# Kernel tuning notes

Measured on AMD Instinct MI355X. Metric: run time of the kernel, lower is better.

## Reference

```python
import jax, jax.numpy as jnp
import numpy as np

N = 100_000      # nodes
E = 1_600_000    # edges (before self loops)
IN = 128         # in_dim
HID = 64         # hidden_dim (per head)
HEADS = 2
NEG_SLOPE = 0.2  # PyG GATConv default negative_slope


def setup_inputs() -> dict:
    key = jax.random.key(0)
    k = jax.random.split(key, 6)
    x = jax.random.normal(k[0], (N, IN), jnp.float32)
    edge_index = jax.random.randint(k[1], (2, E), 0, N, dtype=jnp.int64)
    # GATConv linear (no bias in lin, bias added after aggregation in PyG)
    W = jax.random.normal(k[2], (IN, HEADS * HID), jnp.float32) * (1.0 / np.sqrt(IN))
    att_src = jax.random.normal(k[3], (HEADS, HID), jnp.float32) * 0.1
    att_dst = jax.random.normal(k[4], (HEADS, HID), jnp.float32) * 0.1
    bias = jnp.zeros((HEADS * HID,), jnp.float32)
    prelu_w = jnp.full((HEADS * HID,), 0.25, jnp.float32)  # nn.PReLU default init
    return {"x": x, "edge_index": edge_index, "W": W, "att_src": att_src,
            "att_dst": att_dst, "bias": bias, "prelu_w": prelu_w}


def reference(x, edge_index, W, att_src, att_dst, bias, prelu_w):
    n = x.shape[0]
    h = (x @ W).reshape(n, HEADS, HID)                 # [N,H,C]
    a_s = jnp.einsum('nhc,hc->nh', h, att_src)         # [N,H]
    a_d = jnp.einsum('nhc,hc->nh', h, att_dst)         # [N,H]
    # add self loops (PyG default add_self_loops=True)
    loops = jnp.arange(n, dtype=edge_index.dtype)
    src = jnp.concatenate([edge_index[0], loops])      # [Et]
    dst = jnp.concatenate([edge_index[1], loops])      # [Et]
    logits = a_s[src] + a_d[dst]                       # [Et,H]
    logits = jnp.where(logits >= 0, logits, NEG_SLOPE * logits)  # LeakyReLU
    # segment softmax over destination neighborhoods
    m = jax.ops.segment_max(logits, dst, num_segments=n)         # [N,H]
    e = jnp.exp(logits - m[dst])
    s = jax.ops.segment_sum(e, dst, num_segments=n)              # [N,H]
    alpha = e / (s[dst] + 1e-16)                                 # [Et,H]
    # (attention dropout p=0.2 is identity in eval mode)
    msg = h[src] * alpha[..., None]                    # [Et,H,C]
    out = jax.ops.segment_sum(msg, dst, num_segments=n).reshape(n, HEADS * HID)
    out = out + bias
    # PReLU with per-channel weight
    return jnp.where(out >= 0, out, prelu_w * out)
```

## Files before the change

### kernel.cpp

```cpp
#include <hip/hip_runtime.h>
#include <hip/hip_fp16.h>
#include <hip/hip_bf16.h>
#include <cstdint>
#include <cstddef>

#define NEG_SLOPE 0.2f
#define BSH 8
#define BNODES 256
#define CAP 5120
#define SLOTS 48

typedef __attribute__((ext_vector_type(8))) short short8v;
typedef __attribute__((ext_vector_type(4))) float f32x4;

__device__ __forceinline__ uint32_t bf16pair(float a, float b) {
    __hip_bfloat162 h = __float22bfloat162_rn(make_float2(a, b));
    return *reinterpret_cast<uint32_t*>(&h);
}
__device__ __forceinline__ uint16_t rne16(float f) {
    uint32_t u = __float_as_uint(f);
    return (uint16_t)((u + 0x7fffu + ((u >> 16) & 1u)) >> 16);
}
__device__ __forceinline__ float bflo(uint32_t u) { return __uint_as_float(u << 16); }
__device__ __forceinline__ float bfhi(uint32_t u) { return __uint_as_float(u & 0xffff0000u); }

__global__ __launch_bounds__(256, 3) void gemm_scatter(
    const float* __restrict__ x, const float* __restrict__ W,
    const float* __restrict__ att_src, const float* __restrict__ att_dst,
    uint32_t* __restrict__ hb, float* __restrict__ a_s, float* __restrict__ a_d,
    const int* __restrict__ src, const int* __restrict__ dst,
    int* __restrict__ gcur, uint32_t* __restrict__ pairs,
    int e, int nb, int n, int nbs)
{
    constexpr int PW = 136;
    __shared__ __align__(16) char smem[52224];
    const int tid = threadIdx.x;

    if (blockIdx.x < nbs) {
        int* histL  = (int*)smem;
        int* gbaseL = histL + 512;
        const int t0 = blockIdx.x * 4096;

        for (int i = tid; i < nb; i += 256) histL[i] = 0;
        __syncthreads();

        int      myb[16];
        int      myslot[16];
        uint32_t mypk[16];
#pragma unroll 16
        for (int k = 0; k < 16; ++k) {
            int i = t0 + tid + k * 256;
            if (i < e) {
                int s = __builtin_nontemporal_load(src + i);
                int d = __builtin_nontemporal_load(dst + i);
                int b = d >> BSH;
                myb[k]    = b;
                mypk[k]   = (uint32_t)s | ((uint32_t)(d & (BNODES - 1)) << 17);
                myslot[k] = atomicAdd(&histL[b], 1);
            } else myb[k] = -1;
        }
        __syncthreads();
        for (int i = tid; i < nb; i += 256) {
            int c = histL[i];
            gbaseL[i] = c ? atomicAdd(&gcur[i], c) : 0;
        }
        __syncthreads();
#pragma unroll 16
        for (int k = 0; k < 16; ++k) {
            if (myb[k] >= 0) {
                int p = gbaseL[myb[k]] + myslot[k];
                if (p < CAP) pairs[(size_t)myb[k] * CAP + p] = mypk[k];
            }
        }
        return;
    }

    unsigned short* Wt = (unsigned short*)smem;
    unsigned short* Hs = (unsigned short*)(smem + 34816);
    const int w    = tid >> 6;
    const int lane = tid & 63;
    const int cl   = lane & 15;
    const int gq   = lane >> 4;
    const int base = (blockIdx.x - nbs) * 64;

    const float4* W4 = (const float4*)W;
#pragma unroll
    for (int i = 0; i < 8; ++i) {
        int idx = tid + i * 256;
        int k   = (idx >> 5) * 2, c4 = (idx & 31) * 4;
        float4 v0 = W4[k * 32 + (idx & 31)];
        float4 v1 = W4[(k + 1) * 32 + (idx & 31)];
        *(uint32_t*)&Wt[(c4 + 0) * PW + k] = bf16pair(v0.x, v1.x);
        *(uint32_t*)&Wt[(c4 + 1) * PW + k] = bf16pair(v0.y, v1.y);
        *(uint32_t*)&Wt[(c4 + 2) * PW + k] = bf16pair(v0.z, v1.z);
        *(uint32_t*)&Wt[(c4 + 3) * PW + k] = bf16pair(v0.w, v1.w);
    }

    float asr[8], adr[8];
#pragma unroll
    for (int t = 0; t < 8; ++t) {
        asr[t] = att_src[t * 16 + cl];
        adr[t] = att_dst[t * 16 + cl];
    }
    __syncthreads();

    const int rowg = base + w * 16 + cl;
    const int rowc = rowg < n ? rowg : (n - 1);
    const f32x4* xp = (const f32x4*)(x + (size_t)rowc * 128);

    f32x4 acc[8];
#pragma unroll
    for (int t = 0; t < 8; ++t) acc[t] = (f32x4){0.f, 0.f, 0.f, 0.f};

#pragma unroll
    for (int s = 0; s < 4; ++s) {
        int kq = s * 8 + gq * 2;
        f32x4 f0 = __builtin_nontemporal_load(xp + kq);
        f32x4 f1 = __builtin_nontemporal_load(xp + kq + 1);
        union { short8v v; uint32_t d[4]; } A;
        A.d[0] = bf16pair(f0.x, f0.y);
        A.d[1] = bf16pair(f0.z, f0.w);
        A.d[2] = bf16pair(f1.x, f1.y);
        A.d[3] = bf16pair(f1.z, f1.w);
#pragma unroll
        for (int t = 0; t < 8; ++t) {
            union { short8v v; uint4 q; } B;
            B.q = *(const uint4*)&Wt[(t * 16 + cl) * PW + s * 32 + gq * 8];
            acc[t] = __builtin_amdgcn_mfma_f32_16x16x32_bf16(A.v, B.v, acc[t], 0, 0, 0);
        }
    }

    float ps0[4], ps1[4], pd0[4], pd1[4];
#pragma unroll
    for (int r = 0; r < 4; ++r) { ps0[r] = ps1[r] = pd0[r] = pd1[r] = 0.f; }
#pragma unroll
    for (int t = 0; t < 8; ++t) {
#pragma unroll
        for (int r = 0; r < 4; ++r) {
            float v = acc[t][r];
            if (t < 4) { ps0[r] = fmaf(v, asr[t], ps0[r]); pd0[r] = fmaf(v, adr[t], pd0[r]); }
            else       { ps1[r] = fmaf(v, asr[t], ps1[r]); pd1[r] = fmaf(v, adr[t], pd1[r]); }
        }
    }
#pragma unroll
    for (int off = 1; off < 16; off <<= 1) {
#pragma unroll
        for (int r = 0; r < 4; ++r) {
            ps0[r] += __shfl_xor(ps0[r], off);
            ps1[r] += __shfl_xor(ps1[r], off);
            pd0[r] += __shfl_xor(pd0[r], off);
            pd1[r] += __shfl_xor(pd1[r], off);
        }
    }
    if (cl == 0) {
#pragma unroll
        for (int r = 0; r < 4; ++r) {
            int rg = base + w * 16 + gq * 4 + r;
            if (rg < n) {
                a_s[rg * 2 + 0] = ps0[r]; a_s[rg * 2 + 1] = ps1[r];
                a_d[rg * 2 + 0] = pd0[r]; a_d[rg * 2 + 1] = pd1[r];
            }
        }
    }

#pragma unroll
    for (int t = 0; t < 8; ++t) {
#pragma unroll
        for (int r = 0; r < 4; ++r) {
            int row = gq * 4 + r;
            Hs[(size_t)w * 16 * PW + row * PW + t * 16 + cl] = rne16(acc[t][r]);
        }
    }
    __syncthreads();
#pragma unroll
    for (int q = 0; q < 4; ++q) {
        int row = q * 4 + gq;
        int cu  = 4 * cl;
        uint4 v = *(const uint4*)&Hs[(size_t)w * 16 * PW + row * PW + cu * 2];
        int rg = base + w * 16 + row;
        if (rg < n) *(uint4*)&hb[(size_t)rg * 64 + cu] = v;
    }
}

__global__ __launch_bounds__(512) void build_cols(
    const uint32_t* __restrict__ pairs, const int* __restrict__ gcur,
    uint32_t* __restrict__ meta, uint32_t* __restrict__ cols, int n, int nb)
{
    __shared__ int curL[BNODES];
    const int b = blockIdx.x, tid = threadIdx.x;
    const int nbase = b * BNODES;
    const int nodes = min(BNODES, n - nbase);
    const int C = min(gcur[b], CAP);

    if (tid < BNODES) curL[tid] = 1;
    __syncthreads();
    if (tid < nodes)
        cols[(size_t)(nbase + tid) * SLOTS] = (uint32_t)(nbase + tid);

    for (int i = tid; i < C; i += 512) {
        uint32_t p = __builtin_nontemporal_load(pairs + (size_t)b * CAP + i);
        int dl = p >> 17;
        int s  = p & 0x1FFFF;
        int slot = atomicAdd(&curL[dl], 1);
        if (slot < SLOTS)
            cols[(size_t)(nbase + dl) * SLOTS + slot] = (uint32_t)s;
    }
    __syncthreads();
    if (tid < nodes) meta[nbase + tid] = (uint32_t)min(curL[tid], SLOTS);
}

__global__ __launch_bounds__(256, 8) void attn_agg(
    const uint32_t* __restrict__ hb, const uint32_t* __restrict__ cols,
    const uint32_t* __restrict__ meta,
    const float* __restrict__ a_s, const float* __restrict__ a_d,
    const float* __restrict__ bias, const float* __restrict__ prelu_w,
    float* __restrict__ out, int n)
{
    const int wv   = (blockIdx.x * blockDim.x + threadIdx.x) >> 6;
    const int lane = threadIdx.x & 63;
    const int gwA  = wv * 2;
    if (gwA >= n) return;
    const int h = lane >> 5, hlane = lane & 31;
    const int gw = gwA + h;
    const bool act = gw < n;
    const int deg = act ? (int)meta[gw] : 0;
    const size_t start = (size_t)gw * SLOTS;
    const uint4* hb4 = (const uint4*)hb;

    if (__all(deg <= 32)) {
        float2 ad = make_float2(0.f, 0.f);
        if (act) ad = ((const float2*)a_d)[gw];
        int sv = 0; float e0 = 0.f, e1 = 0.f;
        if (hlane < deg) {
            sv = (int)__builtin_nontemporal_load(cols + start + hlane);
            float2 as = ((const float2*)a_s)[sv];
            float l0 = as.x + ad.x; l0 = l0 >= 0.f ? l0 : NEG_SLOPE * l0;
            float l1 = as.y + ad.y; l1 = l1 >= 0.f ? l1 : NEG_SLOPE * l1;
            e0 = __expf(l0); e1 = __expf(l1);
        }
        float s0 = e0, s1 = e1;
#pragma unroll
        for (int off = 16; off > 0; off >>= 1) {
            s0 += __shfl_xor(s0, off);
            s1 += __shfl_xor(s1, off);
        }
        const float inv0 = 1.f / (s0 + 1e-16f);
        const float inv1 = 1.f / (s1 + 1e-16f);

        const int g = (lane >> 4) & 1, r = lane & 15;
        const int sbase = h * 32;
        float acc[8];
#pragma unroll
        for (int q = 0; q < 8; ++q) acc[q] = 0.f;

        const int iters = (deg + 7) >> 3;
        for (int jj = 0; jj < iters; ++jj) {
            const int j0 = jj * 8 + g * 4;
            int   s0v = __shfl(sv, sbase + j0);
            int   s1v = __shfl(sv, sbase + j0 + 1);
            int   s2v = __shfl(sv, sbase + j0 + 2);
            int   s3v = __shfl(sv, sbase + j0 + 3);
            float A00 = __shfl(e0, sbase + j0),     A10 = __shfl(e1, sbase + j0);
            float A01 = __shfl(e0, sbase + j0 + 1), A11 = __shfl(e1, sbase + j0 + 1);
            float A02 = __shfl(e0, sbase + j0 + 2), A12 = __shfl(e1, sbase + j0 + 2);
            float A03 = __shfl(e0, sbase + j0 + 3), A13 = __shfl(e1, sbase + j0 + 3);
            float Aa = (r < 8) ? A00 : A10;
            float Ab = (r < 8) ? A01 : A11;
            float Ac = (r < 8) ? A02 : A12;
            float Ad = (r < 8) ? A03 : A13;
            uint4 qa = hb4[(size_t)s0v * 16 + r];
            uint4 qb = hb4[(size_t)s1v * 16 + r];
            uint4 qc = hb4[(size_t)s2v * 16 + r];
            uint4 qd = hb4[(size_t)s3v * 16 + r];
            acc[0] = fmaf(Aa, bflo(qa.x), acc[0]); acc[1] = fmaf(Aa, bfhi(qa.x), acc[1]);
            acc[2] = fmaf(Aa, bflo(qa.y), acc[2]); acc[3] = fmaf(Aa, bfhi(qa.y), acc[3]);
            acc[4] = fmaf(Aa, bflo(qa.z), acc[4]); acc[5] = fmaf(Aa, bfhi(qa.z), acc[5]);
            acc[6] = fmaf(Aa, bflo(qa.w), acc[6]); acc[7] = fmaf(Aa, bfhi(qa.w), acc[7]);
            acc[0] = fmaf(Ab, bflo(qb.x), acc[0]); acc[1] = fmaf(Ab, bfhi(qb.x), acc[1]);
            acc[2] = fmaf(Ab, bflo(qb.y), acc[2]); acc[3] = fmaf(Ab, bfhi(qb.y), acc[3]);
            acc[4] = fmaf(Ab, bflo(qb.z), acc[4]); acc[5] = fmaf(Ab, bfhi(qb.z), acc[5]);
            acc[6] = fmaf(Ab, bflo(qb.w), acc[6]); acc[7] = fmaf(Ab, bfhi(qb.w), acc[7]);
            acc[0] = fmaf(Ac, bflo(qc.x), acc[0]); acc[1] = fmaf(Ac, bfhi(qc.x), acc[1]);
            acc[2] = fmaf(Ac, bflo(qc.y), acc[2]); acc[3] = fmaf(Ac, bfhi(qc.y), acc[3]);
            acc[4] = fmaf(Ac, bflo(qc.z), acc[4]); acc[5] = fmaf(Ac, bfhi(qc.z), acc[5]);
            acc[6] = fmaf(Ac, bflo(qc.w), acc[6]); acc[7] = fmaf(Ac, bfhi(qc.w), acc[7]);
            acc[0] = fmaf(Ad, bflo(qd.x), acc[0]); acc[1] = fmaf(Ad, bfhi(qd.x), acc[1]);
            acc[2] = fmaf(Ad, bflo(qd.y), acc[2]); acc[3] = fmaf(Ad, bfhi(qd.y), acc[3]);
            acc[4] = fmaf(Ad, bflo(qd.z), acc[4]); acc[5] = fmaf(Ad, bfhi(qd.z), acc[5]);
            acc[6] = fmaf(Ad, bflo(qd.w), acc[6]); acc[7] = fmaf(Ad, bfhi(qd.w), acc[7]);
        }
#pragma unroll
        for (int q = 0; q < 8; ++q) acc[q] += __shfl_xor(acc[q], 16);

        if (hlane < 16 && act) {
            const float winv = (r < 8) ? inv0 : inv1;
            float4 b0 = ((const float4*)bias)[r * 2];
            float4 b1 = ((const float4*)bias)[r * 2 + 1];
            float4 p0 = ((const float4*)prelu_w)[r * 2];
            float4 p1 = ((const float4*)prelu_w)[r * 2 + 1];
            f32x4 w0, w1;
            w0.x = fmaf(acc[0], winv, b0.x); w0.x = w0.x >= 0.f ? w0.x : p0.x * w0.x;
            w0.y = fmaf(acc[1], winv, b0.y); w0.y = w0.y >= 0.f ? w0.y : p0.y * w0.y;
            w0.z = fmaf(acc[2], winv, b0.z); w0.z = w0.z >= 0.f ? w0.z : p0.z * w0.z;
            w0.w = fmaf(acc[3], winv, b0.w); w0.w = w0.w >= 0.f ? w0.w : p0.w * w0.w;
            w1.x = fmaf(acc[4], winv, b1.x); w1.x = w1.x >= 0.f ? w1.x : p1.x * w1.x;
            w1.y = fmaf(acc[5], winv, b1.y); w1.y = w1.y >= 0.f ? w1.y : p1.y * w1.y;
            w1.z = fmaf(acc[6], winv, b1.z); w1.z = w1.z >= 0.f ? w1.z : p1.z * w1.z;
            w1.w = fmaf(acc[7], winv, b1.w); w1.w = w1.w >= 0.f ? w1.w : p1.w * w1.w;
            float* op = out + (size_t)gw * 128 + r * 8;
            __builtin_nontemporal_store(w0, (f32x4*)op);
            __builtin_nontemporal_store(w1, (f32x4*)(op + 4));
        }
        return;
    }

    for (int pick = 0; pick < 2; ++pick) {
        const int gwp = gwA + pick;
        if (gwp >= n) continue;
        const int dg = (int)meta[gwp];
        const size_t st = (size_t)gwp * SLOTS;
        const float2 ad = ((const float2*)a_d)[gwp];

        int sv = 0; float e0 = 0.f, e1 = 0.f;
        if (lane < dg) {
            sv = (int)cols[st + lane];
            float2 as = ((const float2*)a_s)[sv];
            float l0 = as.x + ad.x; l0 = l0 >= 0.f ? l0 : NEG_SLOPE * l0;
            float l1 = as.y + ad.y; l1 = l1 >= 0.f ? l1 : NEG_SLOPE * l1;
            e0 = __expf(l0); e1 = __expf(l1);
        }
        float s0 = e0, s1 = e1;
#pragma unroll
        for (int off = 32; off > 0; off >>= 1) {
            s0 += __shfl_xor(s0, off);
            s1 += __shfl_xor(s1, off);
        }
        const float inv0 = 1.f / (s0 + 1e-16f);
        const float inv1 = 1.f / (s1 + 1e-16f);
        const int g = lane >> 4, r = lane & 15;
        float acc[8];
#pragma unroll
        for (int q = 0; q < 8; ++q) acc[q] = 0.f;
        const int iters = (dg + 15) >> 4;
        for (int jj = 0; jj < iters; ++jj) {
            const int j0 = jj * 16 + g;
            int   s0v = __shfl(sv, j0);
            int   s1v = __shfl(sv, j0 + 4);
            int   s2v = __shfl(sv, j0 + 8);
            int   s3v = __shfl(sv, j0 + 12);
            float A00 = __shfl(e0, j0),      A10 = __shfl(e1, j0);
            float A01 = __shfl(e0, j0 + 4),  A11 = __shfl(e1, j0 + 4);
            float A02 = __shfl(e0, j0 + 8),  A12 = __shfl(e1, j0 + 8);
            float A03 = __shfl(e0, j0 + 12), A13 = __shfl(e1, j0 + 12);
            float Aa = (r < 8) ? A00 : A10;
            float Ab = (r < 8) ? A01 : A11;
            float Ac = (r < 8) ? A02 : A12;
            float Ad = (r < 8) ? A03 : A13;
            uint4 qa = hb4[(size_t)s0v * 16 + r];
            uint4 qb = hb4[(size_t)s1v * 16 + r];
            uint4 qc = hb4[(size_t)s2v * 16 + r];
            uint4 qd = hb4[(size_t)s3v * 16 + r];
            acc[0] = fmaf(Aa, bflo(qa.x), acc[0]); acc[1] = fmaf(Aa, bfhi(qa.x), acc[1]);
            acc[2] = fmaf(Aa, bflo(qa.y), acc[2]); acc[3] = fmaf(Aa, bfhi(qa.y), acc[3]);
            acc[4] = fmaf(Aa, bflo(qa.z), acc[4]); acc[5] = fmaf(Aa, bfhi(qa.z), acc[5]);
            acc[6] = fmaf(Aa, bflo(qa.w), acc[6]); acc[7] = fmaf(Aa, bfhi(qa.w), acc[7]);
            acc[0] = fmaf(Ab, bflo(qb.x), acc[0]); acc[1] = fmaf(Ab, bfhi(qb.x), acc[1]);
            acc[2] = fmaf(Ab, bflo(qb.y), acc[2]); acc[3] = fmaf(Ab, bfhi(qb.y), acc[3]);
            acc[4] = fmaf(Ab, bflo(qb.z), acc[4]); acc[5] = fmaf(Ab, bfhi(qb.z), acc[5]);
            acc[6] = fmaf(Ab, bflo(qb.w), acc[6]); acc[7] = fmaf(Ab, bfhi(qb.w), acc[7]);
            acc[0] = fmaf(Ac, bflo(qc.x), acc[0]); acc[1] = fmaf(Ac, bfhi(qc.x), acc[1]);
            acc[2] = fmaf(Ac, bflo(qc.y), acc[2]); acc[3] = fmaf(Ac, bfhi(qc.y), acc[3]);
            acc[4] = fmaf(Ac, bflo(qc.z), acc[4]); acc[5] = fmaf(Ac, bfhi(qc.z), acc[5]);
            acc[6] = fmaf(Ac, bflo(qc.w), acc[6]); acc[7] = fmaf(Ac, bfhi(qc.w), acc[7]);
            acc[0] = fmaf(Ad, bflo(qd.x), acc[0]); acc[1] = fmaf(Ad, bfhi(qd.x), acc[1]);
            acc[2] = fmaf(Ad, bflo(qd.y), acc[2]); acc[3] = fmaf(Ad, bfhi(qd.y), acc[3]);
            acc[4] = fmaf(Ad, bflo(qd.z), acc[4]); acc[5] = fmaf(Ad, bfhi(qd.z), acc[5]);
            acc[6] = fmaf(Ad, bflo(qd.w), acc[6]); acc[7] = fmaf(Ad, bfhi(qd.w), acc[7]);
        }
#pragma unroll
        for (int q = 0; q < 8; ++q) {
            acc[q] += __shfl_xor(acc[q], 16);
            acc[q] += __shfl_xor(acc[q], 32);
        }
        if (lane < 16) {
            const float winv = (lane < 8) ? inv0 : inv1;
            float4 b0 = ((const float4*)bias)[lane * 2];
            float4 b1 = ((const float4*)bias)[lane * 2 + 1];
            float4 p0 = ((const float4*)prelu_w)[lane * 2];
            float4 p1 = ((const float4*)prelu_w)[lane * 2 + 1];
            f32x4 w0, w1;
            w0.x = fmaf(acc[0], winv, b0.x); w0.x = w0.x >= 0.f ? w0.x : p0.x * w0.x;
            w0.y = fmaf(acc[1], winv, b0.y); w0.y = w0.y >= 0.f ? w0.y : p0.y * w0.y;
            w0.z = fmaf(acc[2], winv, b0.z); w0.z = w0.z >= 0.f ? w0.z : p0.z * w0.z;
            w0.w = fmaf(acc[3], winv, b0.w); w0.w = w0.w >= 0.f ? w0.w : p0.w * w0.w;
            w1.x = fmaf(acc[4], winv, b1.x); w1.x = w1.x >= 0.f ? w1.x : p1.x * w1.x;
            w1.y = fmaf(acc[5], winv, b1.y); w1.y = w1.y >= 0.f ? w1.y : p1.y * w1.y;
            w1.z = fmaf(acc[6], winv, b1.z); w1.z = w1.z >= 0.f ? w1.z : p1.z * w1.z;
            w1.w = fmaf(acc[7], winv, b1.w); w1.w = w1.w >= 0.f ? w1.w : p1.w * w1.w;
            float* op = out + (size_t)gwp * 128 + lane * 8;
            __builtin_nontemporal_store(w0, (f32x4*)op);
            __builtin_nontemporal_store(w1, (f32x4*)(op + 4));
        }
    }
}

extern "C" void kernel_launch(void* const* d_in, const int* in_sizes, int n_in,
                              void* d_out, int out_size, void* d_ws, size_t ws_size,
                              hipStream_t stream)
{
    const float* x        = (const float*)d_in[0];
    const int*   ei       = (const int*)d_in[1];
    const float* W        = (const float*)d_in[2];
    const float* att_src  = (const float*)d_in[3];
    const float* att_dst  = (const float*)d_in[4];
    const float* bias     = (const float*)d_in[5];
    const float* prelu_w  = (const float*)d_in[6];
    float* out = (float*)d_out;

    const int n = in_sizes[0] / 128;
    const int e = in_sizes[1] / 2;
    const int* srcp = ei;
    const int* dstp = ei + e;
    const int nb  = (n + BNODES - 1) / BNODES;
    const int nbs = (e + 4095) / 4096;
    const int nbg = (n + 63) / 64;

    uint32_t* hb    = (uint32_t*)d_ws;
    uint32_t* meta  = (uint32_t*)(hb + (size_t)n * 64);
    float*    a_s   = (float*)(meta + n);
    float*    a_d   = a_s + (size_t)n * 2;
    int*      gcur  = (int*)(a_d + (size_t)n * 2);
    uint32_t* pairs = (uint32_t*)(gcur + 512);
    uint32_t* cols  = (uint32_t*)(pairs + (size_t)nb * CAP);

    hipMemsetAsync(gcur, 0, 512 * sizeof(int), stream);
    gemm_scatter<<<nbs + nbg, 256, 0, stream>>>(x, W, att_src, att_dst,
                                                hb, a_s, a_d, srcp, dstp,
                                                gcur, pairs, e, nb, n, nbs);
    build_cols<<<nb, 512, 0, stream>>>(pairs, gcur, meta, cols, n, nb);
    const int nwv = (n + 1) / 2;
    attn_agg<<<(nwv + 3) / 4, 256, 0, stream>>>(hb, cols, meta, a_s, a_d,
                                                bias, prelu_w, out, n);
}
```

Baseline: 139.9 us.

## Fuse build_cols into gemm_scatter kernel using a global atomic completion flag

Folds the column-building pass into the combined GEMM/scatter launch as extra trailing blocks. These blocks spin on a global counter that every scatter block increments with release semantics once its pairs are written. The aim is to drop one kernel launch and let column building overlap the GEMM blocks. The cost is spin-waiting blocks that occupy CU slots, which relies on the scatter blocks being scheduled first to avoid deadlock. The build stage also now runs with 256 threads instead of 512.

```diff
diff --git a/kernel.cpp b/kernel.cpp
--- a/kernel.cpp
+++ b/kernel.cpp
@@ -24,13 +24,14 @@
 __device__ __forceinline__ float bflo(uint32_t u) { return __uint_as_float(u << 16); }
 __device__ __forceinline__ float bfhi(uint32_t u) { return __uint_as_float(u & 0xffff0000u); }
 
-__global__ __launch_bounds__(256, 3) void gemm_scatter(
+__global__ __launch_bounds__(256, 3) void gemm_scatter_build(
     const float* __restrict__ x, const float* __restrict__ W,
     const float* __restrict__ att_src, const float* __restrict__ att_dst,
     uint32_t* __restrict__ hb, float* __restrict__ a_s, float* __restrict__ a_d,
     const int* __restrict__ src, const int* __restrict__ dst,
     int* __restrict__ gcur, uint32_t* __restrict__ pairs,
-    int e, int nb, int n, int nbs)
+    uint32_t* __restrict__ meta, uint32_t* __restrict__ cols,
+    int e, int nb, int n, int nbs, int nbg)
 {
     constexpr int PW = 136;
     __shared__ __align__(16) char smem[52224];
@@ -72,6 +73,41 @@
                 if (p < CAP) pairs[(size_t)myb[k] * CAP + p] = mypk[k];
             }
         }
+        __syncthreads();
+        __threadfence();
+        if (tid == 0)
+            __hip_atomic_fetch_add(&gcur[511], 1, __ATOMIC_RELEASE,
+                                   __HIP_MEMORY_SCOPE_AGENT);
+        return;
+    }
+
+    if (blockIdx.x >= nbs + nbg) {
+        int* curL = (int*)smem;
+        const int b = blockIdx.x - nbs - nbg;
+        if (tid == 0) {
+            while (__hip_atomic_load(&gcur[511], __ATOMIC_ACQUIRE,
+                                     __HIP_MEMORY_SCOPE_AGENT) < nbs)
+                __builtin_amdgcn_s_sleep(16);
+        }
+        __syncthreads();
+        __threadfence();
+        const int nbase = b * BNODES;
+        const int nodes = min(BNODES, n - nbase);
+        const int C = min(gcur[b], CAP);
+        curL[tid] = 1;
+        __syncthreads();
+        if (tid < nodes)
+            cols[(size_t)(nbase + tid) * SLOTS] = (uint32_t)(nbase + tid);
+        for (int i = tid; i < C; i += 256) {
+            uint32_t p = pairs[(size_t)b * CAP + i];
+            int dl = p >> 17;
+            int s  = p & 0x1FFFF;
+            int slot = atomicAdd(&curL[dl], 1);
+            if (slot < SLOTS)
+                cols[(size_t)(nbase + dl) * SLOTS + slot] = (uint32_t)s;
+        }
+        __syncthreads();
+        if (tid < nodes) meta[nbase + tid] = (uint32_t)min(curL[tid], SLOTS);
         return;
     }
 
@@ -180,33 +216,6 @@
         int rg = base + w * 16 + row;
         if (rg < n) *(uint4*)&hb[(size_t)rg * 64 + cu] = v;
     }
-}
-
-__global__ __launch_bounds__(512) void build_cols(
-    const uint32_t* __restrict__ pairs, const int* __restrict__ gcur,
-    uint32_t* __restrict__ meta, uint32_t* __restrict__ cols, int n, int nb)
-{
-    __shared__ int curL[BNODES];
-    const int b = blockIdx.x, tid = threadIdx.x;
-    const int nbase = b * BNODES;
-    const int nodes = min(BNODES, n - nbase);
-    const int C = min(gcur[b], CAP);
-
-    if (tid < BNODES) curL[tid] = 1;
-    __syncthreads();
-    if (tid < nodes)
-        cols[(size_t)(nbase + tid) * SLOTS] = (uint32_t)(nbase + tid);
-
-    for (int i = tid; i < C; i += 512) {
-        uint32_t p = __builtin_nontemporal_load(pairs + (size_t)b * CAP + i);
-        int dl = p >> 17;
-        int s  = p & 0x1FFFF;
-        int slot = atomicAdd(&curL[dl], 1);
-        if (slot < SLOTS)
-            cols[(size_t)(nbase + dl) * SLOTS + slot] = (uint32_t)s;
-    }
-    __syncthreads();
-    if (tid < nodes) meta[nbase + tid] = (uint32_t)min(curL[tid], SLOTS);
 }
 
 __global__ __launch_bounds__(256, 8) void attn_agg(
@@ -434,10 +443,9 @@
     uint32_t* cols  = (uint32_t*)(pairs + (size_t)nb * CAP);
 
     hipMemsetAsync(gcur, 0, 512 * sizeof(int), stream);
-    gemm_scatter<<<nbs + nbg, 256, 0, stream>>>(x, W, att_src, att_dst,
-                                                hb, a_s, a_d, srcp, dstp,
-                                                gcur, pairs, e, nb, n, nbs);
-    build_cols<<<nb, 512, 0, stream>>>(pairs, gcur, meta, cols, n, nb);
+    gemm_scatter_build<<<nbs + nbg + nb, 256, 0, stream>>>(
+        x, W, att_src, att_dst, hb, a_s, a_d, srcp, dstp,
+        gcur, pairs, meta, cols, e, nb, n, nbs, nbg);
     const int nwv = (n + 1) / 2;
     attn_agg<<<(nwv + 3) / 4, 256, 0, stream>>>(hb, cols, meta, a_s, a_d,
                                                 bias, prelu_w, out, n);
```

Result: slower. 301.7 us (+115.7%).
